# Optimization experiments

Measured on AMD Instinct MI355X. Metric: run time of the kernel, lower is better.

## Reference

```python
import jax, jax.numpy as jnp
import numpy as np

D_MODEL = 1024
N_HEADS = 16
D_HEAD = D_MODEL // N_HEADS
EPS = 1e-5
ROPE_BASE = 10000.0


def layer_norm(x, w, b=None):
    mu = jnp.mean(x, axis=-1, keepdims=True)
    var = jnp.var(x, axis=-1, keepdims=True)
    y = (x - mu) * jax.lax.rsqrt(var + EPS) * w
    return y + b if b is not None else y


def rope_cos_sin(seq_len, d_head, dtype):
    inv_freq = 1.0 / (ROPE_BASE ** (jnp.arange(0, d_head, 2, dtype=jnp.float32) / d_head))
    t = jnp.arange(seq_len, dtype=jnp.float32)
    freqs = jnp.einsum('l,f->lf', t, inv_freq)          # [L, d_head/2]
    emb = jnp.concatenate([freqs, freqs], axis=-1)       # [L, d_head]
    return jnp.cos(emb).astype(dtype), jnp.sin(emb).astype(dtype)


def rotate_half(x):
    x1, x2 = jnp.split(x, 2, axis=-1)
    return jnp.concatenate([-x2, x1], axis=-1)


def apply_rotary(x, cos, sin):
    # x: [B, L, H, Dh]; cos/sin: [L, Dh]
    c = cos[None, :, None, :]
    s = sin[None, :, None, :]
    return x * c + rotate_half(x) * s


def setup_inputs() -> dict:
    key = jax.random.key(0)
    ks = jax.random.split(key, 8)
    B, L, D = 2, 2048, D_MODEL
    x = jax.random.normal(ks[0], (B, L, D), dtype=jnp.float32)
    seq_id = jnp.sort(jax.random.randint(ks[1], (B, L), 0, 4), axis=-1).astype(jnp.int32)
    scale = 1.0 / np.sqrt(D)
    return {
        'x': x,
        'seq_id': seq_id,
        'ln1_w': jnp.ones((D,), jnp.float32),
        'ln1_b': jnp.zeros((D,), jnp.float32),
        'w_qkv': jax.random.normal(ks[2], (D, 3 * D), jnp.float32) * scale,
        'q_ln_w': jnp.ones((D,), jnp.float32),
        'k_ln_w': jnp.ones((D,), jnp.float32),
        'w_out': jax.random.normal(ks[3], (D, D), jnp.float32) * scale,
    }


def reference(x, seq_id, ln1_w, ln1_b, w_qkv, q_ln_w, k_ln_w, w_out):
    B, L, D = x.shape
    h = layer_norm(x, ln1_w, ln1_b)
    qkv = h @ w_qkv                                    # [B, L, 3D]
    q, k, v = jnp.split(qkv, 3, axis=-1)
    q = layer_norm(q, q_ln_w)                          # qk-LN over full d_model, no bias
    k = layer_norm(k, k_ln_w)
    q = q.reshape(B, L, N_HEADS, D_HEAD)
    k = k.reshape(B, L, N_HEADS, D_HEAD)
    v = v.reshape(B, L, N_HEADS, D_HEAD)
    cos, sin = rope_cos_sin(L, D_HEAD, x.dtype)
    q = apply_rotary(q, cos, sin)
    k = apply_rotary(k, cos, sin)
    scale = 1.0 / np.sqrt(D_HEAD)
    scores = jnp.einsum('bqhd,bkhd->bhqk', q, k) * scale   # [B, H, L, L]
    mask = (seq_id[:, :, None] == seq_id[:, None, :])[:, None, :, :]  # [B,1,L,L]
    scores = jnp.where(mask, scores, jnp.finfo(scores.dtype).min)
    probs = jax.nn.softmax(scores, axis=-1)
    ctx = jnp.einsum('bhqk,bkhd->bqhd', probs, v).reshape(B, L, D)
    return ctx @ w_out
```

## Files before the change

### kernel.cpp

```cpp
#include <hip/hip_runtime.h>
#include <hip/hip_bf16.h>
#include <cstdint>
#include <math.h>

#define LSEQ 2048
#define BATCH 2
#define NHEAD 16
#define DHEAD 64
#define DMODEL 1024
#define ROWS (BATCH*LSEQ)

typedef __bf16 bf16x8 __attribute__((ext_vector_type(8)));
typedef float f32x4 __attribute__((ext_vector_type(4)));
typedef unsigned short u16;

#define GLD(lds_base, src_g) \
  __builtin_amdgcn_global_load_lds((const __attribute__((address_space(1))) void*)(src_g), \
                                   (__attribute__((address_space(3))) void*)(lds_base), 16, 0, 0)
#define VM(n) asm volatile("s_waitcnt vmcnt(" #n ")" ::: "memory")

__device__ __forceinline__ u16 f2bf(float f) {
  unsigned int u = __float_as_uint(f);
  u += 0x7fffu + ((u >> 16) & 1u);
  return (u16)(u >> 16);
}
__device__ __forceinline__ float bf2f(u16 u) {
  return __uint_as_float(((unsigned)u) << 16);
}

__global__ void k_transpose_u16(const u16* __restrict__ in, u16* __restrict__ out) {
  __shared__ u16 tile[32][33];
  int hd = blockIdx.z;
  int l0 = blockIdx.y * 32, d0 = blockIdx.x * 32;
  const u16* ip = in + (size_t)hd * LSEQ * DHEAD;
  u16* op = out + (size_t)hd * LSEQ * DHEAD;
  int tx = threadIdx.x, ty = threadIdx.y;
#pragma unroll
  for (int i = 0; i < 32; i += 8)
    tile[ty + i][tx] = ip[(size_t)(l0 + ty + i) * DHEAD + d0 + tx];
  __syncthreads();
#pragma unroll
  for (int i = 0; i < 32; i += 8)
    op[(size_t)(d0 + ty + i) * LSEQ + l0 + tx] = tile[tx][ty + i];
}

__global__ __launch_bounds__(256) void k_prep(const float* __restrict__ x, const float* __restrict__ ln1w,
                                              const float* __restrict__ ln1b, u16* __restrict__ hbuf,
                                              const float* __restrict__ wqkv, u16* __restrict__ wqkvT,
                                              const float* __restrict__ wout, u16* __restrict__ woutT,
                                              const int* __restrict__ seq, int* __restrict__ bnd,
                                              float* __restrict__ cosb, float* __restrict__ sinb) {
  __shared__ float tile[32][33];
  __shared__ float rb[2][4];
  const int bid = blockIdx.x, t = threadIdx.x;
  if (bid < 4096) {
    const int row = bid;
    const float4 xv = ((const float4*)(x + (size_t)row * DMODEL))[t];
    float s = xv.x + xv.y + xv.z + xv.w;
    float s2 = xv.x * xv.x + xv.y * xv.y + xv.z * xv.z + xv.w * xv.w;
#pragma unroll
    for (int m2 = 1; m2 < 64; m2 <<= 1) { s += __shfl_xor(s, m2); s2 += __shfl_xor(s2, m2); }
    int wv = t >> 6;
    if ((t & 63) == 0) { rb[0][wv] = s; rb[1][wv] = s2; }
    __syncthreads();
    s  = rb[0][0] + rb[0][1] + rb[0][2] + rb[0][3];
    s2 = rb[1][0] + rb[1][1] + rb[1][2] + rb[1][3];
    float mu = s * (1.0f / DMODEL);
    float rs = rsqrtf(s2 * (1.0f / DMODEL) - mu * mu + 1e-5f);
    const float4 wv4 = ((const float4*)ln1w)[t];
    const float4 bv4 = ((const float4*)ln1b)[t];
    ushort4 o;
    o.x = f2bf((xv.x - mu) * rs * wv4.x + bv4.x);
    o.y = f2bf((xv.y - mu) * rs * wv4.y + bv4.y);
    o.z = f2bf((xv.z - mu) * rs * wv4.z + bv4.z);
    o.w = f2bf((xv.w - mu) * rs * wv4.w + bv4.w);
    ((ushort4*)(hbuf + (size_t)row * DMODEL))[t] = o;
  } else if (bid < 4096 + 3072 + 1024) {
    const float* in; u16* out; int R, C, bx, by;
    if (bid < 4096 + 3072) { int rel = bid - 4096; in = wqkv; out = wqkvT; R = 1024; C = 3072; bx = rel % 96; by = rel / 96; }
    else                   { int rel = bid - 7168; in = wout; out = woutT; R = 1024; C = 1024; bx = rel % 32; by = rel / 32; }
    int c0 = bx * 32, r0 = by * 32;
    int tx = t & 31, ty = t >> 5;
#pragma unroll
    for (int i = 0; i < 32; i += 8)
      tile[ty + i][tx] = in[(size_t)(r0 + ty + i) * C + (c0 + tx)];
    __syncthreads();
#pragma unroll
    for (int i = 0; i < 32; i += 8)
      out[(size_t)(c0 + ty + i) * R + (r0 + tx)] = f2bf(tile[tx][ty + i]);
  } else {
    const int rel = bid - 8192;
    if (rel == 0 && t < BATCH * 5) {
      int b = t / 5, s = t % 5;
      const int* row = seq + b * LSEQ;
      int lo = 0, hi = LSEQ;
      while (lo < hi) { int mid = (lo + hi) >> 1; if (row[mid] < s) lo = mid + 1; else hi = mid; }
      bnd[b * 5 + s] = lo;
    }
    int idx = rel * 256 + t;
    if (idx < LSEQ * 32) {
      int l = idx >> 5, f = idx & 31;
      double inv = pow(10000.0, -(double)f / 32.0);
      float ang = (float)l * (float)inv;
      cosb[idx] = cosf(ang);
      sinb[idx] = sinf(ang);
    }
  }
}

template<int OUTMODE>
__global__ __launch_bounds__(512, 4) void k_gemm256(const u16* __restrict__ A, const u16* __restrict__ B,
                                                    void* __restrict__ Cv, int M, int N, int K) {
  __shared__ __align__(16) u16 As[2][128 * 64];
  __shared__ __align__(16) u16 Bs[2][192 * 64];
  const int t = threadIdx.x, lane = t & 63, w = t >> 6;
  const int wr = w >> 2, wc = w & 3;
  const int nbx = N / 192;
  const int nwg = nbx * (M >> 7);
  const int cpx = nwg >> 3;
  const int bid = blockIdx.x;
  const int sw = (bid & 7) * cpx + (bid >> 3);
  const int m0 = (sw / nbx) * 128, n0 = (sw % nbx) * 192;
  const int NT = K >> 6;
  const int cg16 = (lane >> 4) * 16;

  f32x4 acc[4][3] = {};
  bf16x8 af_[2][2], bf_[3][2];
  const u16* Ap = A + (size_t)m0 * K;
  const u16* Bp = B + (size_t)n0 * K;
  const int rr0 = t >> 3;
  const int sz = ((t & 7) * 8) ^ ((rr0 & 7) << 3);
  const u16* pA[2] = { Ap + (size_t)rr0 * K + sz,
                       Ap + (size_t)(rr0 + 64) * K + sz };
  const u16* pB[3] = { Bp + (size_t)rr0 * K + sz,
                       Bp + (size_t)(rr0 + 64) * K + sz,
                       Bp + (size_t)(rr0 + 128) * K + sz };

#define SA1(b, h, EO) GLD((char*)As + (b)*16384 + (h)*8192 + w*1024, pA[h] + (EO))
#define SB3(b, EO) do { \
    GLD((char*)Bs + (b)*24576 +         w*1024, pB[0] + (EO)); \
    GLD((char*)Bs + (b)*24576 +  8192 + w*1024, pB[1] + (EO)); \
    GLD((char*)Bs + (b)*24576 + 16384 + w*1024, pB[2] + (EO)); \
  } while (0)

#define READ_AF(asb, mh) do { \
    _Pragma("unroll") for (int i2 = 0; i2 < 2; i2++) { \
      const int rowA = (((mh)*2 + i2)*2 + wr)*16 + (lane & 15); \
      const int sA = (rowA & 7) << 4; \
      _Pragma("unroll") for (int kk = 0; kk < 2; kk++) \
        af_[i2][kk] = *(const bf16x8*)((const char*)(asb) + (rowA & 63)*128 + ((kk*64 + cg16) ^ sA)); \
    } } while (0)
#define READ_BF(bsb) do { \
    _Pragma("unroll") for (int j2 = 0; j2 < 3; j2++) { \
      const int rowB = (j2*4 + wc)*16 + (lane & 15); \
      const int sB = (rowB & 7) << 4; \
      _Pragma("unroll") for (int kk = 0; kk < 2; kk++) \
        bf_[j2][kk] = *(const bf16x8*)((const char*)(bsb) + rowB*128 + ((kk*64 + cg16) ^ sB)); \
    } } while (0)
#define MFMA12(mh) do { \
    _Pragma("unroll") for (int kk = 0; kk < 2; kk++) \
      _Pragma("unroll") for (int i2 = 0; i2 < 2; i2++) \
        _Pragma("unroll") for (int j2 = 0; j2 < 3; j2++) \
          acc[(mh)*2+i2][j2] = __builtin_amdgcn_mfma_f32_16x16x32_bf16( \
              af_[i2][kk], bf_[j2][kk], acc[(mh)*2+i2][j2], 0, 0, 0); \
  } while (0)

  SA1(0, 0, 0); SA1(0, 1, 0); SB3(0, 0);
  SA1(1, 0, 64);
  VM(1);
  __builtin_amdgcn_s_barrier();

  const char* a0  = (const char*)As;
  const char* a0h = a0 + 8192;
  const char* a1  = a0 + 16384;
  const char* a1h = a0 + 24576;
  const char* b0  = (const char*)Bs;
  const char* b1  = b0 + 24576;
  const int NIT = NT >> 1;
  for (int i = 0; i < NIT; i++) {
    const bool lst = (i == NIT - 1);
    READ_AF(a0, 0); READ_BF(b0);
    SA1(1, 1, 64); SB3(1, 64);
    __builtin_amdgcn_s_barrier();
    asm volatile("s_waitcnt lgkmcnt(0)" ::: "memory");
    __builtin_amdgcn_s_setprio(1); MFMA12(0); __builtin_amdgcn_s_setprio(0);
    __builtin_amdgcn_s_barrier();
    READ_AF(a0h, 1);
    if (!lst) SA1(0, 0, 128);
    __builtin_amdgcn_s_barrier();
    asm volatile("s_waitcnt lgkmcnt(0)" ::: "memory");
    __builtin_amdgcn_s_setprio(1); MFMA12(1); __builtin_amdgcn_s_setprio(0);
    if (lst) VM(0); else VM(1);
    __builtin_amdgcn_s_barrier();
    READ_AF(a1, 0); READ_BF(b1);
    if (!lst) { SA1(0, 1, 128); SB3(0, 128); }
    __builtin_amdgcn_s_barrier();
    asm volatile("s_waitcnt lgkmcnt(0)" ::: "memory");
    __builtin_amdgcn_s_setprio(1); MFMA12(0); __builtin_amdgcn_s_setprio(0);
    __builtin_amdgcn_s_barrier();
    READ_AF(a1h, 1);
    if (!lst) SA1(1, 0, 192);
    __builtin_amdgcn_s_barrier();
    asm volatile("s_waitcnt lgkmcnt(0)" ::: "memory");
    __builtin_amdgcn_s_setprio(1); MFMA12(1); __builtin_amdgcn_s_setprio(0);
    if (!lst) VM(1);
    __builtin_amdgcn_s_barrier();
    pA[0] += 128; pA[1] += 128;
    pB[0] += 128; pB[1] += 128; pB[2] += 128;
  }
#undef MFMA12
#undef READ_BF
#undef READ_AF
#undef SA1
#undef SB3

  const int cr = (lane >> 4) * 4, cc = lane & 15;
#pragma unroll
  for (int fi = 0; fi < 4; fi++)
#pragma unroll
    for (int fj = 0; fj < 3; fj++) {
      const size_t roff = (size_t)(m0 + (fi * 2 + wr) * 16 + cr) * N + (n0 + (fj * 4 + wc) * 16 + cc);
      if (OUTMODE == 0) {
        float* Cp = (float*)Cv + roff;
#pragma unroll
        for (int r = 0; r < 4; r++) Cp[(size_t)r * N] = acc[fi][fj][r];
      } else {
        u16* Cp = (u16*)Cv + roff;
#pragma unroll
        for (int r = 0; r < 4; r++) Cp[(size_t)r * N] = f2bf(acc[fi][fj][r]);
      }
    }
}

template<int OUTMODE>
__global__ __launch_bounds__(256) void k_gemm_bt(const u16* __restrict__ A, const u16* __restrict__ B,
                                                 void* __restrict__ Cv, int M, int N, int K) {
  __shared__ __align__(16) u16 As[2][128 * 64];
  __shared__ __align__(16) u16 Bs[2][128 * 64];
  const int t = threadIdx.x;
  const int lane = t & 63, w = t >> 6;
  const int nbx = N >> 7;
  const int nwg = nbx * (M >> 7);
  const int cpx = nwg >> 3;
  const int bid = blockIdx.x;
  const int sw = (bid & 7) * cpx + (bid >> 3);
  const int m0 = (sw / nbx) * 128, n0 = (sw % nbx) * 128;
  const int wm = (w >> 1) * 64, wn = (w & 1) * 64;
  const int NT = K >> 6;
  f32x4 acc[4][4] = {};
  const u16* Ap = A + (size_t)m0 * K;
  const u16* Bp = B + (size_t)n0 * K;
  const int cr0 = lane >> 3, cs = lane & 7;

#define GSTAGE(bb, kt_) do { \
    _Pragma("unroll") \
    for (int s2 = 0; s2 < 4; s2++) { \
      int ch = w * 4 + s2; \
      int row = ch * 8 + cr0; \
      int cb = cs ^ (row & 7); \
      GLD((char*)As[bb] + ch * 1024, Ap + (size_t)row * K + (kt_) * 64 + cb * 8); \
      GLD((char*)Bs[bb] + ch * 1024, Bp + (size_t)row * K + (kt_) * 64 + cb * 8); \
    } } while (0)

  GSTAGE(0, 0);
  VM(0);
  __builtin_amdgcn_s_barrier();
  int cur = 0;
  for (int kt = 0; kt < NT; kt++) {
    if (kt + 1 < NT) GSTAGE(cur ^ 1, kt + 1);
    const u16* asb = As[cur];
    const u16* bsb = Bs[cur];
#pragma unroll
    for (int kk = 0; kk < 2; kk++) {
      bf16x8 af[4], bfr[4];
#pragma unroll
      for (int i = 0; i < 4; i++) {
        int rowa = wm + i * 16 + (lane & 15);
        af[i] = *(const bf16x8*)((const char*)asb + rowa * 128 + ((kk * 64 + (lane >> 4) * 16) ^ ((rowa & 7) << 4)));
        int rowb = wn + i * 16 + (lane & 15);
        bfr[i] = *(const bf16x8*)((const char*)bsb + rowb * 128 + ((kk * 64 + (lane >> 4) * 16) ^ ((rowb & 7) << 4)));
      }
#pragma unroll
      for (int mf = 0; mf < 4; mf++)
#pragma unroll
        for (int nf = 0; nf < 4; nf++)
          acc[mf][nf] = __builtin_amdgcn_mfma_f32_16x16x32_bf16(af[mf], bfr[nf], acc[mf][nf], 0, 0, 0);
    }
    VM(0);
    __builtin_amdgcn_s_barrier();
    cur ^= 1;
  }
#undef GSTAGE
  const int cr = (lane >> 4) * 4, cc = lane & 15;
#pragma unroll
  for (int mf = 0; mf < 4; mf++)
#pragma unroll
    for (int nf = 0; nf < 4; nf++) {
      if (OUTMODE == 0) {
        float* Cp = (float*)Cv + (size_t)(m0 + wm + mf * 16 + cr) * N + (n0 + wn + nf * 16 + cc);
#pragma unroll
        for (int r = 0; r < 4; r++) Cp[(size_t)r * N] = acc[mf][nf][r];
      } else {
        u16* Cp = (u16*)Cv + (size_t)(m0 + wm + mf * 16 + cr) * N + (n0 + wn + nf * 16 + cc);
#pragma unroll
        for (int r = 0; r < 4; r++) Cp[(size_t)r * N] = f2bf(acc[mf][nf][r]);
      }
    }
}

__global__ __launch_bounds__(256) void k_qk_ln_rope(const u16* __restrict__ qkv,
                                                    const float* __restrict__ qw, const float* __restrict__ kw,
                                                    const float* __restrict__ cosb, const float* __restrict__ sinb,
                                                    u16* __restrict__ Q, u16* __restrict__ K, u16* __restrict__ V) {
  int row = blockIdx.x, t = threadIdx.x;
  int b = row >> 11, l = row & 2047;
  const u16* base = qkv + (size_t)row * 3072;
  ushort4 qu = ((const ushort4*)base)[t];
  ushort4 ku = ((const ushort4*)(base + 1024))[t];
  ushort4 vu = ((const ushort4*)(base + 2048))[t];
  float qx = bf2f(qu.x), qy = bf2f(qu.y), qz = bf2f(qu.z), qw_ = bf2f(qu.w);
  float kx = bf2f(ku.x), ky = bf2f(ku.y), kz = bf2f(ku.z), kw_ = bf2f(ku.w);
  float red[4];
  red[0] = qx + qy + qz + qw_;
  red[1] = qx * qx + qy * qy + qz * qz + qw_ * qw_;
  red[2] = kx + ky + kz + kw_;
  red[3] = kx * kx + ky * ky + kz * kz + kw_ * kw_;
#pragma unroll
  for (int i = 0; i < 4; i++)
#pragma unroll
    for (int m2 = 1; m2 < 64; m2 <<= 1) red[i] += __shfl_xor(red[i], m2);
  __shared__ float rb[4][4];
  int w = t >> 6;
  if ((t & 63) == 0) { rb[w][0] = red[0]; rb[w][1] = red[1]; rb[w][2] = red[2]; rb[w][3] = red[3]; }
  __syncthreads();
  float S1 = rb[0][0] + rb[1][0] + rb[2][0] + rb[3][0];
  float S2 = rb[0][1] + rb[1][1] + rb[2][1] + rb[3][1];
  float S3 = rb[0][2] + rb[1][2] + rb[2][2] + rb[3][2];
  float S4 = rb[0][3] + rb[1][3] + rb[2][3] + rb[3][3];
  float muq = S1 * (1.0f / DMODEL), rsq = rsqrtf(S2 * (1.0f / DMODEL) - muq * muq + 1e-5f);
  float muk = S3 * (1.0f / DMODEL), rsk = rsqrtf(S4 * (1.0f / DMODEL) - muk * muk + 1e-5f);
  __shared__ float qs[1024], ks[1024];
  float4 qwv = ((const float4*)qw)[t];
  float4 kwv = ((const float4*)kw)[t];
  qs[t * 4 + 0] = (qx - muq) * rsq * qwv.x;  ks[t * 4 + 0] = (kx - muk) * rsk * kwv.x;
  qs[t * 4 + 1] = (qy - muq) * rsq * qwv.y;  ks[t * 4 + 1] = (ky - muk) * rsk * kwv.y;
  qs[t * 4 + 2] = (qz - muq) * rsq * qwv.z;  ks[t * 4 + 2] = (kz - muk) * rsk * kwv.z;
  qs[t * 4 + 3] = (qw_ - muq) * rsq * qwv.w; ks[t * 4 + 3] = (kw_ - muk) * rsk * kwv.w;
  __syncthreads();
  int d0 = t * 4;
  int hh = d0 >> 6;
  union { ushort4 v4; u16 e[4]; } qo, ko;
#pragma unroll
  for (int i = 0; i < 4; i++) {
    int d = d0 + i, dd = d & 63, fr = dd & 31;
    float c = cosb[l * 32 + fr], s = sinb[l * 32 + fr];
    float q1 = qs[d], q2 = (dd < 32) ? -qs[d + 32] : qs[d - 32];
    float k1 = ks[d], k2 = (dd < 32) ? -ks[d + 32] : ks[d - 32];
    qo.e[i] = f2bf(q1 * c + q2 * s);
    ko.e[i] = f2bf(k1 * c + k2 * s);
  }
  size_t oidx = ((size_t)(b * NHEAD + hh) * LSEQ + l) * DHEAD + (d0 & 63);
  *(ushort4*)(Q + oidx) = qo.v4;
  *(ushort4*)(K + oidx) = ko.v4;
  *(ushort4*)(V + oidx) = vu;
}

__global__ __launch_bounds__(512) void k_attn(const u16* __restrict__ Q, const u16* __restrict__ Kb,
                                              const u16* __restrict__ VTb, const int* __restrict__ seq,
                                              const int* __restrict__ bnd, u16* __restrict__ ctx) {
  __shared__ __align__(16) u16 Ks[2][64 * 64];
  __shared__ __align__(16) u16 Vs[2][64 * 64];
  __shared__ __align__(16) u16 Pw[8][16 * 64];

  const int bid = blockIdx.x;
  const int sw = (bid & 7) * 64 + (bid >> 3);
  const int qt = sw & 15, h = (sw >> 4) & 15, b = sw >> 8;
  const int t = threadIdx.x, l = t & 63, w = t >> 6;
  const int c = l & 15, g = l >> 4;
  const int q0 = qt * 128;
  const size_t hoff = (size_t)(b * NHEAD + h) * LSEQ * DHEAD;
  const u16* Qg = Q + hoff;
  const u16* Kg = Kb + hoff;
  const u16* Vg = VTb + hoff;
  const int* seqb = seq + b * LSEQ;
  const int* bnd5 = bnd + b * 5;

  const int qw0 = q0 + w * 16;
  const int myq = qw0 + c;
  const int sq = seqb[myq];
  const int lo = bnd5[sq], hi = bnd5[sq + 1];
  const int wlo = bnd5[seqb[qw0]];
  const int whi = bnd5[seqb[qw0 + 15] + 1];
  int kbeg = bnd5[seqb[q0]] & ~63;
  int kend = (bnd5[seqb[q0 + 127] + 1] + 63) & ~63;
  if (kend > LSEQ) kend = LSEQ;

  bf16x8 qf[2];
  qf[0] = *(const bf16x8*)(Qg + (size_t)myq * 64 + g * 8);
  qf[1] = *(const bf16x8*)(Qg + (size_t)myq * 64 + 32 + g * 8);

  f32x4 acc[4] = {};
  float lsum = 0.f;

  const int rr = t >> 3;
  const int szk = ((t & 7) * 8) ^ ((rr & 7) << 3);
  const u16* pK = Kg + (size_t)rr * 64 + szk;
  const u16* pV = Vg + (size_t)rr * LSEQ + szk;

#define STAGE(bb, kt_) do { \
    GLD((char*)Ks[bb] + w * 1024, pK + (size_t)(kt_) * 64); \
    GLD((char*)Vs[bb] + w * 1024, pV + (kt_)); \
  } while (0)

  STAGE(0, kbeg);
  int cur = 0;
  for (int kt = kbeg; kt < kend; kt += 64) {
    const bool more = (kt + 64) < kend;
    if (more) STAGE(cur ^ 1, kt + 64);
    if (more) VM(2);
    else      VM(0);
    __builtin_amdgcn_s_barrier();
    __builtin_amdgcn_sched_barrier(0);
    if (kt < whi && kt + 64 > wlo) {
      const u16* ksb = Ks[cur];
      const u16* vsb = Vs[cur];
      f32x4 st[4] = {};
#pragma unroll
      for (int kk = 0; kk < 2; kk++) {
        bf16x8 kf[4];
#pragma unroll
        for (int i = 0; i < 4; i++) {
          int row = i * 16 + c;
          kf[i] = *(const bf16x8*)((const char*)ksb + row * 128 + ((kk * 64 + g * 16) ^ ((row & 7) << 4)));
        }
#pragma unroll
        for (int i = 0; i < 4; i++)
          st[i] = __builtin_amdgcn_mfma_f32_16x16x32_bf16(kf[i], qf[kk], st[i], 0, 0, 0);
      }
      const int kb0 = kt + g * 4;
#pragma unroll
      for (int i = 0; i < 4; i++) {
        float p[4];
#pragma unroll
        for (int r = 0; r < 4; r++) {
          int kglob = kb0 + i * 16 + r;
          bool ok = ((unsigned)(kglob - lo)) < ((unsigned)(hi - lo));
          float x = ok ? fmaf(st[i][r], 0.125f, -8.0f) : -1e30f;
          p[r] = __expf(x);
          lsum += p[r];
        }
        unsigned w0, w1;
        asm("v_cvt_pk_bf16_f32 %0, %1, %2" : "=v"(w0) : "v"(p[0]), "v"(p[1]));
        asm("v_cvt_pk_bf16_f32 %0, %1, %2" : "=v"(w1) : "v"(p[2]), "v"(p[3]));
        uint2 wp; wp.x = w0; wp.y = w1;
        *(uint2*)((char*)Pw[w] + c * 128 + ((i * 32 + g * 8) ^ ((c & 7) << 4))) = wp;
      }
#pragma unroll
      for (int kk = 0; kk < 2; kk++) {
        bf16x8 pa = *(const bf16x8*)((char*)Pw[w] + c * 128 + ((kk * 64 + g * 16) ^ ((c & 7) << 4)));
        bf16x8 vf[4];
#pragma unroll
        for (int df = 0; df < 4; df++) {
          int row = df * 16 + c;
          vf[df] = *(const bf16x8*)((const char*)vsb + row * 128 + ((kk * 64 + g * 16) ^ ((row & 7) << 4)));
        }
#pragma unroll
        for (int df = 0; df < 4; df++)
          acc[df] = __builtin_amdgcn_mfma_f32_16x16x32_bf16(pa, vf[df], acc[df], 0, 0, 0);
      }
    }
    __builtin_amdgcn_sched_barrier(0);
    __builtin_amdgcn_s_barrier();
    cur ^= 1;
  }
#undef STAGE

  lsum += __shfl_xor(lsum, 16);
  lsum += __shfl_xor(lsum, 32);
#pragma unroll
  for (int r = 0; r < 4; r++) {
    float lr = __shfl(lsum, g * 4 + r, 64);
    float rls = 1.0f / lr;
    int qrow = qw0 + g * 4 + r;
    u16* op = ctx + (size_t)(b * LSEQ + qrow) * DMODEL + h * 64 + c;
#pragma unroll
    for (int df = 0; df < 4; df++)
      op[df * 16] = f2bf(acc[df][r] * rls);
  }
}

extern "C" void kernel_launch(void* const* d_in, const int* in_sizes, int n_in,
                              void* d_out, int out_size, void* d_ws, size_t ws_size,
                              hipStream_t stream) {
  const float* x    = (const float*)d_in[0];
  const int*   seq  = (const int*)d_in[1];
  const float* ln1w = (const float*)d_in[2];
  const float* ln1b = (const float*)d_in[3];
  const float* wqkv = (const float*)d_in[4];
  const float* qlnw = (const float*)d_in[5];
  const float* klnw = (const float*)d_in[6];
  const float* wout = (const float*)d_in[7];
  float* out = (float*)d_out;

  char* p = (char*)d_ws;
  u16* wqkvT = (u16*)p;  p += (size_t)3072 * 1024 * 2;
  u16* woutT = (u16*)p;  p += (size_t)1024 * 1024 * 2;
  u16* hbuf  = (u16*)p;  p += (size_t)ROWS * DMODEL * 2;
  u16* Qb    = (u16*)p;  p += (size_t)ROWS * DMODEL * 2;
  u16* Kbuf  = (u16*)p;  p += (size_t)ROWS * DMODEL * 2;
  u16* Vbuf  = (u16*)p;  p += (size_t)ROWS * DMODEL * 2;
  u16* VTbuf = (u16*)p;  p += (size_t)ROWS * DMODEL * 2;
  u16* ctxb  = (u16*)p;  p += (size_t)ROWS * DMODEL * 2;
  float* cosb = (float*)p; p += (size_t)LSEQ * 32 * 4;
  float* sinb = (float*)p; p += (size_t)LSEQ * 32 * 4;
  int* bnd   = (int*)p;  p += 256;
  u16* qkv   = (u16*)p;  p += (size_t)ROWS * 3072 * 2;

  k_prep<<<8448, 256, 0, stream>>>(x, ln1w, ln1b, hbuf, wqkv, wqkvT, wout, woutT, seq, bnd, cosb, sinb);
  k_gemm256<1><<<(ROWS / 128) * (3072 / 192), 512, 0, stream>>>(hbuf, wqkvT, (void*)qkv, ROWS, 3072, 1024);
  k_qk_ln_rope<<<ROWS, 256, 0, stream>>>(qkv, qlnw, klnw, cosb, sinb, Qb, Kbuf, Vbuf);
  k_transpose_u16<<<dim3(DHEAD / 32, LSEQ / 32, BATCH * NHEAD), dim3(32, 8), 0, stream>>>(Vbuf, VTbuf);
  k_attn<<<BATCH * NHEAD * (LSEQ / 128), 512, 0, stream>>>(Qb, Kbuf, VTbuf, seq, bnd, ctxb);
  k_gemm_bt<0><<<(ROWS / 128) * (1024 / 128), 256, 0, stream>>>(ctxb, woutT, (void*)out, ROWS, 1024, 1024);
}
```

Baseline: 112.3 us.

## Fuse V transpose into qk-LN/RoPE kernel and pipeline gemm_bt loads

The separate V write and transpose kernel are removed. Extra blocks in the qk-LN/RoPE kernel now transpose V straight from the qkv buffer into VT, which saves one launch and one round trip of V through global memory. The k_gemm_bt loop also moves its vmcnt wait to just after issuing the next stage, waiting only on the current tile, so global-to-LDS prefetch overlaps the MFMA work. The transpose reads use a stride of 3072 elements, which may coalesce less well than before.

```diff
diff --git a/kernel.cpp b/kernel.cpp
--- a/kernel.cpp
+++ b/kernel.cpp
@@ -26,22 +26,6 @@
 }
 __device__ __forceinline__ float bf2f(u16 u) {
   return __uint_as_float(((unsigned)u) << 16);
-}
-
-__global__ void k_transpose_u16(const u16* __restrict__ in, u16* __restrict__ out) {
-  __shared__ u16 tile[32][33];
-  int hd = blockIdx.z;
-  int l0 = blockIdx.y * 32, d0 = blockIdx.x * 32;
-  const u16* ip = in + (size_t)hd * LSEQ * DHEAD;
-  u16* op = out + (size_t)hd * LSEQ * DHEAD;
-  int tx = threadIdx.x, ty = threadIdx.y;
-#pragma unroll
-  for (int i = 0; i < 32; i += 8)
-    tile[ty + i][tx] = ip[(size_t)(l0 + ty + i) * DHEAD + d0 + tx];
-  __syncthreads();
-#pragma unroll
-  for (int i = 0; i < 32; i += 8)
-    op[(size_t)(d0 + ty + i) * LSEQ + l0 + tx] = tile[tx][ty + i];
 }
 
 __global__ __launch_bounds__(256) void k_prep(const float* __restrict__ x, const float* __restrict__ ln1w,
@@ -263,11 +247,11 @@
     } } while (0)
 
   GSTAGE(0, 0);
-  VM(0);
-  __builtin_amdgcn_s_barrier();
   int cur = 0;
   for (int kt = 0; kt < NT; kt++) {
-    if (kt + 1 < NT) GSTAGE(cur ^ 1, kt + 1);
+    if (kt + 1 < NT) { GSTAGE(cur ^ 1, kt + 1); VM(8); }
+    else             { VM(0); }
+    __builtin_amdgcn_s_barrier();
     const u16* asb = As[cur];
     const u16* bsb = Bs[cur];
 #pragma unroll
@@ -286,7 +270,6 @@
         for (int nf = 0; nf < 4; nf++)
           acc[mf][nf] = __builtin_amdgcn_mfma_f32_16x16x32_bf16(af[mf], bfr[nf], acc[mf][nf], 0, 0, 0);
     }
-    VM(0);
     __builtin_amdgcn_s_barrier();
     cur ^= 1;
   }
@@ -308,61 +291,79 @@
     }
 }
 
-__global__ __launch_bounds__(256) void k_qk_ln_rope(const u16* __restrict__ qkv,
-                                                    const float* __restrict__ qw, const float* __restrict__ kw,
-                                                    const float* __restrict__ cosb, const float* __restrict__ sinb,
-                                                    u16* __restrict__ Q, u16* __restrict__ K, u16* __restrict__ V) {
-  int row = blockIdx.x, t = threadIdx.x;
-  int b = row >> 11, l = row & 2047;
-  const u16* base = qkv + (size_t)row * 3072;
-  ushort4 qu = ((const ushort4*)base)[t];
-  ushort4 ku = ((const ushort4*)(base + 1024))[t];
-  ushort4 vu = ((const ushort4*)(base + 2048))[t];
-  float qx = bf2f(qu.x), qy = bf2f(qu.y), qz = bf2f(qu.z), qw_ = bf2f(qu.w);
-  float kx = bf2f(ku.x), ky = bf2f(ku.y), kz = bf2f(ku.z), kw_ = bf2f(ku.w);
-  float red[4];
-  red[0] = qx + qy + qz + qw_;
-  red[1] = qx * qx + qy * qy + qz * qz + qw_ * qw_;
-  red[2] = kx + ky + kz + kw_;
-  red[3] = kx * kx + ky * ky + kz * kz + kw_ * kw_;
-#pragma unroll
-  for (int i = 0; i < 4; i++)
-#pragma unroll
-    for (int m2 = 1; m2 < 64; m2 <<= 1) red[i] += __shfl_xor(red[i], m2);
-  __shared__ float rb[4][4];
-  int w = t >> 6;
-  if ((t & 63) == 0) { rb[w][0] = red[0]; rb[w][1] = red[1]; rb[w][2] = red[2]; rb[w][3] = red[3]; }
-  __syncthreads();
-  float S1 = rb[0][0] + rb[1][0] + rb[2][0] + rb[3][0];
-  float S2 = rb[0][1] + rb[1][1] + rb[2][1] + rb[3][1];
-  float S3 = rb[0][2] + rb[1][2] + rb[2][2] + rb[3][2];
-  float S4 = rb[0][3] + rb[1][3] + rb[2][3] + rb[3][3];
-  float muq = S1 * (1.0f / DMODEL), rsq = rsqrtf(S2 * (1.0f / DMODEL) - muq * muq + 1e-5f);
-  float muk = S3 * (1.0f / DMODEL), rsk = rsqrtf(S4 * (1.0f / DMODEL) - muk * muk + 1e-5f);
-  __shared__ float qs[1024], ks[1024];
-  float4 qwv = ((const float4*)qw)[t];
-  float4 kwv = ((const float4*)kw)[t];
-  qs[t * 4 + 0] = (qx - muq) * rsq * qwv.x;  ks[t * 4 + 0] = (kx - muk) * rsk * kwv.x;
-  qs[t * 4 + 1] = (qy - muq) * rsq * qwv.y;  ks[t * 4 + 1] = (ky - muk) * rsk * kwv.y;
-  qs[t * 4 + 2] = (qz - muq) * rsq * qwv.z;  ks[t * 4 + 2] = (kz - muk) * rsk * kwv.z;
-  qs[t * 4 + 3] = (qw_ - muq) * rsq * qwv.w; ks[t * 4 + 3] = (kw_ - muk) * rsk * kwv.w;
-  __syncthreads();
-  int d0 = t * 4;
-  int hh = d0 >> 6;
-  union { ushort4 v4; u16 e[4]; } qo, ko;
-#pragma unroll
-  for (int i = 0; i < 4; i++) {
-    int d = d0 + i, dd = d & 63, fr = dd & 31;
-    float c = cosb[l * 32 + fr], s = sinb[l * 32 + fr];
-    float q1 = qs[d], q2 = (dd < 32) ? -qs[d + 32] : qs[d - 32];
-    float k1 = ks[d], k2 = (dd < 32) ? -ks[d + 32] : ks[d - 32];
-    qo.e[i] = f2bf(q1 * c + q2 * s);
-    ko.e[i] = f2bf(k1 * c + k2 * s);
+__global__ __launch_bounds__(256) void k_qkv_post(const u16* __restrict__ qkv,
+                                                  const float* __restrict__ qw, const float* __restrict__ kw,
+                                                  const float* __restrict__ cosb, const float* __restrict__ sinb,
+                                                  u16* __restrict__ Q, u16* __restrict__ K, u16* __restrict__ VT) {
+  const int bid = blockIdx.x, t = threadIdx.x;
+  if (bid < 4096) {
+    __shared__ float qs[1024], ks[1024];
+    __shared__ float rb[4][4];
+    int row = bid;
+    int b = row >> 11, l = row & 2047;
+    const u16* base = qkv + (size_t)row * 3072;
+    ushort4 qu = ((const ushort4*)base)[t];
+    ushort4 ku = ((const ushort4*)(base + 1024))[t];
+    float qx = bf2f(qu.x), qy = bf2f(qu.y), qz = bf2f(qu.z), qw_ = bf2f(qu.w);
+    float kx = bf2f(ku.x), ky = bf2f(ku.y), kz = bf2f(ku.z), kw_ = bf2f(ku.w);
+    float red[4];
+    red[0] = qx + qy + qz + qw_;
+    red[1] = qx * qx + qy * qy + qz * qz + qw_ * qw_;
+    red[2] = kx + ky + kz + kw_;
+    red[3] = kx * kx + ky * ky + kz * kz + kw_ * kw_;
+#pragma unroll
+    for (int i = 0; i < 4; i++)
+#pragma unroll
+      for (int m2 = 1; m2 < 64; m2 <<= 1) red[i] += __shfl_xor(red[i], m2);
+    int w = t >> 6;
+    if ((t & 63) == 0) { rb[w][0] = red[0]; rb[w][1] = red[1]; rb[w][2] = red[2]; rb[w][3] = red[3]; }
+    __syncthreads();
+    float S1 = rb[0][0] + rb[1][0] + rb[2][0] + rb[3][0];
+    float S2 = rb[0][1] + rb[1][1] + rb[2][1] + rb[3][1];
+    float S3 = rb[0][2] + rb[1][2] + rb[2][2] + rb[3][2];
+    float S4 = rb[0][3] + rb[1][3] + rb[2][3] + rb[3][3];
+    float muq = S1 * (1.0f / DMODEL), rsq = rsqrtf(S2 * (1.0f / DMODEL) - muq * muq + 1e-5f);
+    float muk = S3 * (1.0f / DMODEL), rsk = rsqrtf(S4 * (1.0f / DMODEL) - muk * muk + 1e-5f);
+    float4 qwv = ((const float4*)qw)[t];
+    float4 kwv = ((const float4*)kw)[t];
+    qs[t * 4 + 0] = (qx - muq) * rsq * qwv.x;  ks[t * 4 + 0] = (kx - muk) * rsk * kwv.x;
+    qs[t * 4 + 1] = (qy - muq) * rsq * qwv.y;  ks[t * 4 + 1] = (ky - muk) * rsk * kwv.y;
+    qs[t * 4 + 2] = (qz - muq) * rsq * qwv.z;  ks[t * 4 + 2] = (kz - muk) * rsk * kwv.z;
+    qs[t * 4 + 3] = (qw_ - muq) * rsq * qwv.w; ks[t * 4 + 3] = (kw_ - muk) * rsk * kwv.w;
+    __syncthreads();
+    int d0 = t * 4;
+    int hh = d0 >> 6;
+    union { ushort4 v4; u16 e[4]; } qo, ko;
+#pragma unroll
+    for (int i = 0; i < 4; i++) {
+      int d = d0 + i, dd = d & 63, fr = dd & 31;
+      float c = cosb[l * 32 + fr], s = sinb[l * 32 + fr];
+      float q1 = qs[d], q2 = (dd < 32) ? -qs[d + 32] : qs[d - 32];
+      float k1 = ks[d], k2 = (dd < 32) ? -ks[d + 32] : ks[d - 32];
+      qo.e[i] = f2bf(q1 * c + q2 * s);
+      ko.e[i] = f2bf(k1 * c + k2 * s);
+    }
+    size_t oidx = ((size_t)(b * NHEAD + hh) * LSEQ + l) * DHEAD + (d0 & 63);
+    *(ushort4*)(Q + oidx) = qo.v4;
+    *(ushort4*)(K + oidx) = ko.v4;
+  } else {
+    __shared__ u16 vtile[32][33];
+    const int rel = bid - 4096;
+    const int hd = rel >> 7;
+    const int tl = rel & 127;
+    const int d0 = (tl & 1) * 32, l0 = (tl >> 1) * 32;
+    const int gl = (hd >> 4) * LSEQ;
+    const u16* ip = qkv + (size_t)(gl + l0) * 3072 + 2048 + (hd & 15) * 64 + d0;
+    u16* op = VT + (size_t)hd * LSEQ * DHEAD + (size_t)d0 * LSEQ + l0;
+    int tx = t & 31, ty = t >> 5;
+#pragma unroll
+    for (int i = 0; i < 32; i += 8)
+      vtile[ty + i][tx] = ip[(size_t)(ty + i) * 3072 + tx];
+    __syncthreads();
+#pragma unroll
+    for (int i = 0; i < 32; i += 8)
+      op[(size_t)(ty + i) * LSEQ + tx] = vtile[tx][ty + i];
   }
-  size_t oidx = ((size_t)(b * NHEAD + hh) * LSEQ + l) * DHEAD + (d0 & 63);
-  *(ushort4*)(Q + oidx) = qo.v4;
-  *(ushort4*)(K + oidx) = ko.v4;
-  *(ushort4*)(V + oidx) = vu;
 }
 
 __global__ __launch_bounds__(512) void k_attn(const u16* __restrict__ Q, const u16* __restrict__ Kb,
@@ -508,7 +509,6 @@
   u16* hbuf  = (u16*)p;  p += (size_t)ROWS * DMODEL * 2;
   u16* Qb    = (u16*)p;  p += (size_t)ROWS * DMODEL * 2;
   u16* Kbuf  = (u16*)p;  p += (size_t)ROWS * DMODEL * 2;
-  u16* Vbuf  = (u16*)p;  p += (size_t)ROWS * DMODEL * 2;
   u16* VTbuf = (u16*)p;  p += (size_t)ROWS * DMODEL * 2;
   u16* ctxb  = (u16*)p;  p += (size_t)ROWS * DMODEL * 2;
   float* cosb = (float*)p; p += (size_t)LSEQ * 32 * 4;
@@ -518,8 +518,7 @@
 
   k_prep<<<8448, 256, 0, stream>>>(x, ln1w, ln1b, hbuf, wqkv, wqkvT, wout, woutT, seq, bnd, cosb, sinb);
   k_gemm256<1><<<(ROWS / 128) * (3072 / 192), 512, 0, stream>>>(hbuf, wqkvT, (void*)qkv, ROWS, 3072, 1024);
-  k_qk_ln_rope<<<ROWS, 256, 0, stream>>>(qkv, qlnw, klnw, cosb, sinb, Qb, Kbuf, Vbuf);
-  k_transpose_u16<<<dim3(DHEAD / 32, LSEQ / 32, BATCH * NHEAD), dim3(32, 8), 0, stream>>>(Vbuf, VTbuf);
+  k_qkv_post<<<8192, 256, 0, stream>>>(qkv, qlnw, klnw, cosb, sinb, Qb, Kbuf, VTbuf);
   k_attn<<<BATCH * NHEAD * (LSEQ / 128), 512, 0, stream>>>(Qb, Kbuf, VTbuf, seq, bnd, ctxb);
   k_gemm_bt<0><<<(ROWS / 128) * (1024 / 128), 256, 0, stream>>>(ctxb, woutT, (void*)out, ROWS, 1024, 1024);
 }
```

Result: faster. 107.5 us (-4.2%).
